# Kernel optimization log

Measured on AMD Instinct MI355X. Metric: run time of the kernel, lower is better.

## Reference

```python
import jax, jax.numpy as jnp
import numpy as np
from jax import lax

B, T, V, D, H, C = 256, 1024, 5000, 100, 64, 2


def setup_inputs() -> dict:
    key = jax.random.key(0)
    k0, k1, k2, k3, k4 = jax.random.split(key, 5)
    tokens = jax.random.randint(k0, (B, T), 0, V)  # 0 is the mask/pad id
    E = jax.random.normal(k1, (V, D), dtype=jnp.float32) * 0.05
    W = jax.random.normal(k2, (D, H), dtype=jnp.float32) * (1.0 / np.sqrt(D))
    U = jax.random.normal(k3, (H, H), dtype=jnp.float32) * (1.0 / np.sqrt(H))
    b = jnp.zeros((H,), dtype=jnp.float32)
    Wd = jax.random.normal(k4, (H, C), dtype=jnp.float32) * (1.0 / np.sqrt(H))
    bd = jnp.zeros((C,), dtype=jnp.float32)
    return {"tokens": tokens, "E": E, "W": W, "U": U, "b": b, "Wd": Wd, "bd": bd}


def reference(tokens, E, W, U, b, Wd, bd):
    # Embedding with mask_zero=True: mask where token != 0
    x = E[tokens]                      # [B, T, D]
    mask = tokens != 0                 # [B, T] bool
    # Precompute input projection for all timesteps (batched GEMM).
    xW = jnp.einsum('btd,dh->bth', x, W) + b  # [B, T, H]

    def step(h, inp):
        xw_t, m_t = inp                # xw_t: [B,H], m_t: [B]
        h_new = jnp.tanh(xw_t + h @ U)
        # Keras masked recurrence: masked steps carry previous state/output.
        h = jnp.where(m_t[:, None], h_new, h)
        return h, h

    h0 = jnp.zeros((tokens.shape[0], U.shape[0]), dtype=xW.dtype)
    _, hs = lax.scan(step, h0, (jnp.swapaxes(xW, 0, 1), mask.T))  # hs: [T, B, H]
    hs = jnp.swapaxes(hs, 0, 1)        # [B, T, H]
    pooled = jnp.mean(hs, axis=1)      # tf.reduce_mean over time (unmasked mean)
    # Dropout is identity at inference.
    logits = pooled @ Wd + bd
    return jax.nn.sigmoid(logits)
```

## Files before the change

### kernel.cpp

```cpp
#include <hip/hip_runtime.h>

#define B_ 256
#define T_ 1024
#define V_ 5000
#define D_ 100
#define H_ 64
#define C_ 2

typedef float f32x4 __attribute__((ext_vector_type(4)));

#define SCALE_ 2.885390081777927f

__global__ __launch_bounds__(256) void ew_kernel(const float* __restrict__ E,
                                                 const float* __restrict__ W,
                                                 const float* __restrict__ bias,
                                                 float* __restrict__ EW) {
    int idx = blockIdx.x * 256 + threadIdx.x;
    if (idx >= V_ * H_) return;
    int h = idx & (H_ - 1);
    int v = idx >> 6;
    float acc = bias[h];
    const float* Erow = E + v * D_;
    #pragma unroll 4
    for (int d = 0; d < D_; ++d) {
        acc = fmaf(Erow[d], W[d * H_ + h], acc);
    }
    EW[idx] = SCALE_ * acc;
}

__device__ __forceinline__ float readlane_f(float v, int lane) {
    return __uint_as_float(__builtin_amdgcn_readlane(__float_as_uint(v), lane));
}

__global__ __launch_bounds__(64, 1) void rnn_kernel(const int* __restrict__ tokens,
                                                    const float* __restrict__ EW,
                                                    const float* __restrict__ U,
                                                    const float* __restrict__ Wd,
                                                    const float* __restrict__ bd,
                                                    float* __restrict__ out) {
    const int b = blockIdx.x;
    const int j = threadIdx.x;

    __shared__ int sh_tok[T_ + 2];

    f32x4 uq[16];
    #pragma unroll
    for (int c = 0; c < 16; ++c) {
        uq[c][0] = SCALE_ * U[(4 * c + 0) * H_ + j];
        uq[c][1] = SCALE_ * U[(4 * c + 1) * H_ + j];
        uq[c][2] = SCALE_ * U[(4 * c + 2) * H_ + j];
        uq[c][3] = SCALE_ * U[(4 * c + 3) * H_ + j];
    }
    asm volatile("" : "+v"(uq[0]), "+v"(uq[1]), "+v"(uq[2]), "+v"(uq[3]),
                      "+v"(uq[4]), "+v"(uq[5]), "+v"(uq[6]), "+v"(uq[7]),
                      "+v"(uq[8]), "+v"(uq[9]), "+v"(uq[10]), "+v"(uq[11]),
                      "+v"(uq[12]), "+v"(uq[13]), "+v"(uq[14]), "+v"(uq[15]));

    const int* tok = tokens + b * T_;
    #pragma unroll
    for (int k = 0; k < T_ / H_; ++k) {
        sh_tok[k * H_ + j] = tok[k * H_ + j];
    }
    if (j < 2) sh_tok[T_ + j] = 0;
    __syncthreads();

    float h = 0.f;
    float pooled = 0.f;

    int2 tkA = *(const int2*)&sh_tok[0];
    float xw0 = EW[tkA.x * H_ + j];
    float xw1 = EW[tkA.y * H_ + j];

    #define DOT_GROUP(g)                                                 \
    {                                                                    \
        float s0 = readlane_f(h, 8 * (g) + 0);                           \
        float s1 = readlane_f(h, 8 * (g) + 1);                           \
        float s2 = readlane_f(h, 8 * (g) + 2);                           \
        float s3 = readlane_f(h, 8 * (g) + 3);                           \
        float s4 = readlane_f(h, 8 * (g) + 4);                           \
        float s5 = readlane_f(h, 8 * (g) + 5);                           \
        float s6 = readlane_f(h, 8 * (g) + 6);                           \
        float s7 = readlane_f(h, 8 * (g) + 7);                           \
        asm volatile("" : "+s"(s0), "+s"(s1), "+s"(s2), "+s"(s3),        \
                          "+s"(s4), "+s"(s5), "+s"(s6), "+s"(s7));       \
        a0 = fmaf(s0, uq[2 * (g) + 0][0], a0);                           \
        a1 = fmaf(s1, uq[2 * (g) + 0][1], a1);                           \
        a2 = fmaf(s2, uq[2 * (g) + 0][2], a2);                           \
        a3 = fmaf(s3, uq[2 * (g) + 0][3], a3);                           \
        a0 = fmaf(s4, uq[2 * (g) + 1][0], a0);                           \
        a1 = fmaf(s5, uq[2 * (g) + 1][1], a1);                           \
        a2 = fmaf(s6, uq[2 * (g) + 1][2], a2);                           \
        a3 = fmaf(s7, uq[2 * (g) + 1][3], a3);                           \
    }

    #define RNN_STEP(tokv, xwv)                                          \
    {                                                                    \
        float a0 = (xwv), a1 = 0.f, a2 = 0.f, a3 = 0.f;                  \
        DOT_GROUP(0) DOT_GROUP(1) DOT_GROUP(2) DOT_GROUP(3)              \
        DOT_GROUP(4) DOT_GROUP(5) DOT_GROUP(6) DOT_GROUP(7)              \
        float x2 = (a0 + a1) + (a2 + a3);                                \
        float ef = __builtin_amdgcn_exp2f(x2);                           \
        float r = __builtin_amdgcn_rcpf(ef + 1.f);                       \
        float hn = fmaf(-2.f, r, 1.f);                                   \
        h = ((tokv) != 0) ? hn : h;                                      \
        pooled += h;                                                     \
    }

    for (int t = 0; t < T_; t += 2) {
        asm volatile("" :: "v"(uq[0]), "v"(uq[1]), "v"(uq[2]), "v"(uq[3]),
                           "v"(uq[4]), "v"(uq[5]), "v"(uq[6]), "v"(uq[7]),
                           "v"(uq[8]), "v"(uq[9]), "v"(uq[10]), "v"(uq[11]),
                           "v"(uq[12]), "v"(uq[13]), "v"(uq[14]), "v"(uq[15]));

        int2 tkB = *(const int2*)&sh_tok[t + 2];
        float xw2 = EW[tkB.x * H_ + j];
        float xw3 = EW[tkB.y * H_ + j];

        RNN_STEP(tkA.x, xw0);
        RNN_STEP(tkA.y, xw1);

        tkA = tkB;
        xw0 = xw2;
        xw1 = xw3;
    }
    #undef RNN_STEP
    #undef DOT_GROUP

    float p = pooled * (1.0f / (float)T_);
    float v0 = p * Wd[j * C_ + 0];
    float v1 = p * Wd[j * C_ + 1];
    #pragma unroll
    for (int off = 32; off >= 1; off >>= 1) {
        v0 += __shfl_down(v0, off, 64);
        v1 += __shfl_down(v1, off, 64);
    }
    if (j == 0) {
        float l0 = v0 + bd[0];
        float l1 = v1 + bd[1];
        out[b * C_ + 0] = 1.f / (1.f + __expf(-l0));
        out[b * C_ + 1] = 1.f / (1.f + __expf(-l1));
    }
}

extern "C" void kernel_launch(void* const* d_in, const int* in_sizes, int n_in,
                              void* d_out, int out_size, void* d_ws, size_t ws_size,
                              hipStream_t stream) {
    const int*   tokens = (const int*)  d_in[0];
    const float* E      = (const float*)d_in[1];
    const float* W      = (const float*)d_in[2];
    const float* U      = (const float*)d_in[3];
    const float* bias   = (const float*)d_in[4];
    const float* Wd     = (const float*)d_in[5];
    const float* bd     = (const float*)d_in[6];
    float* out = (float*)d_out;
    float* EW  = (float*)d_ws;

    ew_kernel<<<(V_ * H_ + 255) / 256, 256, 0, stream>>>(E, W, bias, EW);
    rnn_kernel<<<B_, H_, 0, stream>>>(tokens, EW, U, Wd, bd, out);
}
```

Baseline: 318.7 us.

## Split hidden-state broadcast between readlane and LDS vector reads

The per-step h broadcast is split: the first 32 hidden values still go through v_readlane into scalar registers, while the other 32 are written to shared memory and read back as broadcast 128-bit LDS loads. The LDS traffic is meant to overlap with the readlane/FMA chain and halve the serialized readlane work on the critical recurrent path. Sched group barriers are added to order the LDS write and reads. The added LDS round trip adds latency, and with a single wavefront there is no barrier, which relies on wave-level execution order for correctness.

New measurement: 450.4 us. 41.3% more time.

```diff
diff --git a/kernel.cpp b/kernel.cpp
--- a/kernel.cpp
+++ b/kernel.cpp
@@ -42,19 +42,21 @@
     const int j = threadIdx.x;
 
     __shared__ int sh_tok[T_ + 2];
-
-    f32x4 uq[16];
+    __shared__ alignas(16) float sh_hb[H_];
+
+    f32x4 uqR[8], uqL[8];
     #pragma unroll
-    for (int c = 0; c < 16; ++c) {
-        uq[c][0] = SCALE_ * U[(4 * c + 0) * H_ + j];
-        uq[c][1] = SCALE_ * U[(4 * c + 1) * H_ + j];
-        uq[c][2] = SCALE_ * U[(4 * c + 2) * H_ + j];
-        uq[c][3] = SCALE_ * U[(4 * c + 3) * H_ + j];
-    }
-    asm volatile("" : "+v"(uq[0]), "+v"(uq[1]), "+v"(uq[2]), "+v"(uq[3]),
-                      "+v"(uq[4]), "+v"(uq[5]), "+v"(uq[6]), "+v"(uq[7]),
-                      "+v"(uq[8]), "+v"(uq[9]), "+v"(uq[10]), "+v"(uq[11]),
-                      "+v"(uq[12]), "+v"(uq[13]), "+v"(uq[14]), "+v"(uq[15]));
+    for (int g = 0; g < 8; ++g) {
+        #pragma unroll
+        for (int i = 0; i < 4; ++i) {
+            uqR[g][i] = SCALE_ * U[(4 * g + i) * H_ + j];
+            uqL[g][i] = SCALE_ * U[(32 + 4 * g + i) * H_ + j];
+        }
+    }
+    asm volatile("" : "+v"(uqR[0]), "+v"(uqR[1]), "+v"(uqR[2]), "+v"(uqR[3]),
+                      "+v"(uqR[4]), "+v"(uqR[5]), "+v"(uqR[6]), "+v"(uqR[7]),
+                      "+v"(uqL[0]), "+v"(uqL[1]), "+v"(uqL[2]), "+v"(uqL[3]),
+                      "+v"(uqL[4]), "+v"(uqL[5]), "+v"(uqL[6]), "+v"(uqL[7]));
 
     const int* tok = tokens + b * T_;
     #pragma unroll
@@ -71,7 +73,7 @@
     float xw0 = EW[tkA.x * H_ + j];
     float xw1 = EW[tkA.y * H_ + j];
 
-    #define DOT_GROUP(g)                                                 \
+    #define RL_GROUP(g)                                                  \
     {                                                                    \
         float s0 = readlane_f(h, 8 * (g) + 0);                           \
         float s1 = readlane_f(h, 8 * (g) + 1);                           \
@@ -83,21 +85,63 @@
         float s7 = readlane_f(h, 8 * (g) + 7);                           \
         asm volatile("" : "+s"(s0), "+s"(s1), "+s"(s2), "+s"(s3),        \
                           "+s"(s4), "+s"(s5), "+s"(s6), "+s"(s7));       \
-        a0 = fmaf(s0, uq[2 * (g) + 0][0], a0);                           \
-        a1 = fmaf(s1, uq[2 * (g) + 0][1], a1);                           \
-        a2 = fmaf(s2, uq[2 * (g) + 0][2], a2);                           \
-        a3 = fmaf(s3, uq[2 * (g) + 0][3], a3);                           \
-        a0 = fmaf(s4, uq[2 * (g) + 1][0], a0);                           \
-        a1 = fmaf(s5, uq[2 * (g) + 1][1], a1);                           \
-        a2 = fmaf(s6, uq[2 * (g) + 1][2], a2);                           \
-        a3 = fmaf(s7, uq[2 * (g) + 1][3], a3);                           \
+        a0 = fmaf(s0, uqR[2 * (g) + 0][0], a0);                          \
+        a1 = fmaf(s1, uqR[2 * (g) + 0][1], a1);                          \
+        a0 = fmaf(s2, uqR[2 * (g) + 0][2], a0);                          \
+        a1 = fmaf(s3, uqR[2 * (g) + 0][3], a1);                          \
+        a0 = fmaf(s4, uqR[2 * (g) + 1][0], a0);                          \
+        a1 = fmaf(s5, uqR[2 * (g) + 1][1], a1);                          \
+        a0 = fmaf(s6, uqR[2 * (g) + 1][2], a0);                          \
+        a1 = fmaf(s7, uqR[2 * (g) + 1][3], a1);                          \
     }
 
     #define RNN_STEP(tokv, xwv)                                          \
     {                                                                    \
+        sh_hb[j] = h;                                                    \
+        f32x4 hv0 = *(const f32x4*)&sh_hb[32];                           \
+        f32x4 hv1 = *(const f32x4*)&sh_hb[36];                           \
+        f32x4 hv2 = *(const f32x4*)&sh_hb[40];                           \
+        f32x4 hv3 = *(const f32x4*)&sh_hb[44];                           \
+        f32x4 hv4 = *(const f32x4*)&sh_hb[48];                           \
+        f32x4 hv5 = *(const f32x4*)&sh_hb[52];                           \
+        f32x4 hv6 = *(const f32x4*)&sh_hb[56];                           \
+        f32x4 hv7 = *(const f32x4*)&sh_hb[60];                           \
+        __builtin_amdgcn_sched_group_barrier(0x200, 1, 0); \
+        __builtin_amdgcn_sched_group_barrier(0x100, 8, 0); \
         float a0 = (xwv), a1 = 0.f, a2 = 0.f, a3 = 0.f;                  \
-        DOT_GROUP(0) DOT_GROUP(1) DOT_GROUP(2) DOT_GROUP(3)              \
-        DOT_GROUP(4) DOT_GROUP(5) DOT_GROUP(6) DOT_GROUP(7)              \
+        RL_GROUP(0) RL_GROUP(1) RL_GROUP(2) RL_GROUP(3)                  \
+        a2 = fmaf(hv0[0], uqL[0][0], a2);                                \
+        a3 = fmaf(hv0[1], uqL[0][1], a3);                                \
+        a2 = fmaf(hv0[2], uqL[0][2], a2);                                \
+        a3 = fmaf(hv0[3], uqL[0][3], a3);                                \
+        a2 = fmaf(hv1[0], uqL[1][0], a2);                                \
+        a3 = fmaf(hv1[1], uqL[1][1], a3);                                \
+        a2 = fmaf(hv1[2], uqL[1][2], a2);                                \
+        a3 = fmaf(hv1[3], uqL[1][3], a3);                                \
+        a2 = fmaf(hv2[0], uqL[2][0], a2);                                \
+        a3 = fmaf(hv2[1], uqL[2][1], a3);                                \
+        a2 = fmaf(hv2[2], uqL[2][2], a2);                                \
+        a3 = fmaf(hv2[3], uqL[2][3], a3);                                \
+        a2 = fmaf(hv3[0], uqL[3][0], a2);                                \
+        a3 = fmaf(hv3[1], uqL[3][1], a3);                                \
+        a2 = fmaf(hv3[2], uqL[3][2], a2);                                \
+        a3 = fmaf(hv3[3], uqL[3][3], a3);                                \
+        a2 = fmaf(hv4[0], uqL[4][0], a2);                                \
+        a3 = fmaf(hv4[1], uqL[4][1], a3);                                \
+        a2 = fmaf(hv4[2], uqL[4][2], a2);                                \
+        a3 = fmaf(hv4[3], uqL[4][3], a3);                                \
+        a2 = fmaf(hv5[0], uqL[5][0], a2);                                \
+        a3 = fmaf(hv5[1], uqL[5][1], a3);                                \
+        a2 = fmaf(hv5[2], uqL[5][2], a2);                                \
+        a3 = fmaf(hv5[3], uqL[5][3], a3);                                \
+        a2 = fmaf(hv6[0], uqL[6][0], a2);                                \
+        a3 = fmaf(hv6[1], uqL[6][1], a3);                                \
+        a2 = fmaf(hv6[2], uqL[6][2], a2);                                \
+        a3 = fmaf(hv6[3], uqL[6][3], a3);                                \
+        a2 = fmaf(hv7[0], uqL[7][0], a2);                                \
+        a3 = fmaf(hv7[1], uqL[7][1], a3);                                \
+        a2 = fmaf(hv7[2], uqL[7][2], a2);                                \
+        a3 = fmaf(hv7[3], uqL[7][3], a3);                                \
         float x2 = (a0 + a1) + (a2 + a3);                                \
         float ef = __builtin_amdgcn_exp2f(x2);                           \
         float r = __builtin_amdgcn_rcpf(ef + 1.f);                       \
@@ -107,10 +151,10 @@
     }
 
     for (int t = 0; t < T_; t += 2) {
-        asm volatile("" :: "v"(uq[0]), "v"(uq[1]), "v"(uq[2]), "v"(uq[3]),
-                           "v"(uq[4]), "v"(uq[5]), "v"(uq[6]), "v"(uq[7]),
-                           "v"(uq[8]), "v"(uq[9]), "v"(uq[10]), "v"(uq[11]),
-                           "v"(uq[12]), "v"(uq[13]), "v"(uq[14]), "v"(uq[15]));
+        asm volatile("" :: "v"(uqR[0]), "v"(uqR[1]), "v"(uqR[2]), "v"(uqR[3]),
+                           "v"(uqR[4]), "v"(uqR[5]), "v"(uqR[6]), "v"(uqR[7]),
+                           "v"(uqL[0]), "v"(uqL[1]), "v"(uqL[2]), "v"(uqL[3]),
+                           "v"(uqL[4]), "v"(uqL[5]), "v"(uqL[6]), "v"(uqL[7]));
 
         int2 tkB = *(const int2*)&sh_tok[t + 2];
         float xw2 = EW[tkB.x * H_ + j];
@@ -124,7 +168,7 @@
         xw1 = xw3;
     }
     #undef RNN_STEP
-    #undef DOT_GROUP
+    #undef RL_GROUP
 
     float p = pooled * (1.0f / (float)T_);
     float v0 = p * Wd[j * C_ + 0];
```
